# Kernel tuning notes

Measured on AMD Instinct MI355X. Metric: run time of the kernel, lower is better.

## Reference

```python
import jax, jax.numpy as jnp
import numpy as np

B, S, H, STATIC = 128, 128, 256, 2
BLOCKS = S // 2            # rotate_types = 2 for block_dim=2, allow_rot=True
DYN = 3 * BLOCKS           # dynamic channels: move / rotate_small / rotate_large


def setup_inputs() -> dict:
    key = jax.random.key(0)
    ks = jax.random.split(key, 16)
    p = lambda k, shape: (jax.random.normal(k, shape, jnp.float32) * 0.1)
    return {
        "static": jax.random.normal(ks[0], (B, STATIC + 1, S), jnp.float32),
        "dynamic": jnp.zeros((B, DYN, S), jnp.float32),
        "decoder_input": jax.random.normal(ks[1], (B, STATIC, 1), jnp.float32),
        # static/dynamic/decoder 1x1 conv encoders (weight [H, C_in], bias [H])
        "enc_s_W": p(ks[2], (H, STATIC)), "enc_s_b": p(ks[3], (H,)),
        "enc_d_W": p(ks[4], (H, DYN)),    "enc_d_b": p(ks[5], (H,)),
        "dec_W": p(ks[6], (H, STATIC)),   "dec_b": p(ks[7], (H,)),
        # single-layer GRU (torch layout: [3H, H] gates r,z,n)
        "gru_W_ih": p(ks[8], (3 * H, H)), "gru_W_hh": p(ks[9], (3 * H, H)),
        "gru_b_ih": p(ks[10], (3 * H,)),  "gru_b_hh": p(ks[11], (3 * H,)),
        # encoder attention and pointer heads: v [H], W [H, 3H]
        "attn_v": p(ks[12], (H,)), "attn_W": p(ks[13], (H, 3 * H)),
        "ptr_v": p(ks[14], (H,)),  "ptr_W": p(ks[15], (H, 3 * H)),
    }


def reference(static, dynamic, decoder_input,
              enc_s_W, enc_s_b, enc_d_W, enc_d_b, dec_W, dec_b,
              gru_W_ih, gru_W_hh, gru_b_ih, gru_b_hh,
              attn_v, attn_W, ptr_v, ptr_W):
    static_part = static[:, 1:, :]                                  # [B, STATIC, S]
    static_h = jnp.einsum('hi,bis->bhs', enc_s_W, static_part) + enc_s_b[None, :, None]
    dynamic_h = jnp.einsum('hi,bis->bhs', enc_d_W, dynamic) + enc_d_b[None, :, None]

    # initial mask from dynamic state (move + rotate feasibility)
    bn = dynamic.shape[1] // 3
    move = dynamic[:, :bn, :].sum(1)
    dyn_mask = dynamic[:, bn:2 * bn, :].sum(1) * dynamic[:, 2 * bn:3 * bn, :].sum(1) + move
    logmask = jnp.where(dyn_mask != 0, -jnp.inf, 0.0)               # log(current_mask), [B, S]

    hsz = gru_W_hh.shape[1]
    h0 = jnp.zeros((static.shape[0], hsz), static.dtype)            # GRU default zero state

    def gru_cell(x, h):
        gi = x @ gru_W_ih.T + gru_b_ih
        gh = h @ gru_W_hh.T + gru_b_hh
        ir, iz, inn = jnp.split(gi, 3, -1)
        hr, hz, hn = jnp.split(gh, 3, -1)
        r = jax.nn.sigmoid(ir + hr)
        z = jax.nn.sigmoid(iz + hz)
        n = jnp.tanh(inn + r * hn)
        return (1.0 - z) * n + z * h

    def step(carry, _):
        h_prev, dec_in = carry
        dec_h = jnp.einsum('hi,bi->bh', dec_W, dec_in[:, :, 0]) + dec_b   # decoder 1x1 conv
        h = gru_cell(dec_h, h_prev)                                       # rnn_out == new hidden
        rnn_b = jnp.broadcast_to(h[:, :, None], static_h.shape)
        hid = jnp.concatenate([static_h, dynamic_h, rnn_b], axis=1)       # [B, 3H, S]
        attn = jax.nn.softmax(
            jnp.einsum('h,bhs->bs', attn_v,
                       jnp.tanh(jnp.einsum('hk,bks->bhs', attn_W, hid))), axis=-1)
        context = jnp.einsum('bs,bhs->bh', attn, static_h)
        ctx_b = jnp.broadcast_to(context[:, :, None], static_h.shape)
        energy = jnp.concatenate([static_h, dynamic_h, ctx_b], axis=1)    # [B, 3H, S]
        logits = jnp.einsum('h,bhs->bs', ptr_v,
                            jnp.tanh(jnp.einsum('hk,bks->bhs', ptr_W, energy)))
        probs = jax.nn.softmax(logits + logmask, axis=-1)                 # [B, S]
        ptr = jnp.argmax(probs, axis=1)                                   # greedy (eval mode)
        logp = jnp.log(jnp.max(probs, axis=1))
        new_dec = jax.lax.stop_gradient(
            jnp.take_along_axis(static_part, ptr[:, None, None], axis=2))  # [B, STATIC, 1]
        return (h, new_dec), (ptr, logp)

    (_, _), (ptrs, logps) = jax.lax.scan(step, (h0, decoder_input), None,
                                         length=static_part.shape[2])
    tour_idx = ptrs.T    # [B, S]
    tour_logp = logps.T  # [B, S]
    return tour_idx, tour_logp
```

## Files before the change

### kernel.cpp

```cpp
#include <hip/hip_runtime.h>
#include <hip/hip_bf16.h>
#include <math.h>

#define BB   128
#define SS   128
#define HH   256
#define DYNN 192

#define OFF_FLAG  0
#define OFF_G     64
#define OFF_G0    (OFF_G + 1536)
#define OFF_M1A   (OFF_G0 + 768)
#define OFF_CA    (OFF_M1A + 512)
#define OFF_M1P   (OFF_CA + 256)
#define OFF_CP    (OFF_M1P + 512)
#define OFF_M3P   (OFF_CP + 256)
#define OFF_CP3   (OFF_M3P + 512)
#define OFF_LM    (OFF_CP3 + 256)
#define OFF_M2A   (OFF_LM + 16384)
#define OFF_M2P   (OFF_M2A + 49152)
#define OFF_BASEA (OFF_M2P + 49152)
#define OFF_BASEP (OFF_BASEA + 4194304)
#define OFF_END   (OFF_BASEP + 4194304)

__device__ __forceinline__ float tanh_fast(float x) {
    float e = __builtin_amdgcn_exp2f(x * 2.885390081777927f);
    return 1.0f - 2.0f * __builtin_amdgcn_rcpf(e + 1.0f);
}

__global__ void k1_logmask(const float* __restrict__ dyn, float* __restrict__ lm,
                           int* __restrict__ flag) {
    int g = blockIdx.x * 256 + threadIdx.x;
    if (g >= BB * SS) return;
    int b = g >> 7, s = g & 127;
    const float* p = dyn + (size_t)b * DYNN * SS + s;
    float mv = 0.f, m1 = 0.f, m2 = 0.f;
    bool nz = false;
    for (int i = 0; i < 64; ++i)        { float v = p[(size_t)i * SS]; mv += v; nz |= (v != 0.f); }
    for (int i = 64; i < 128; ++i)      { float v = p[(size_t)i * SS]; m1 += v; nz |= (v != 0.f); }
    for (int i = 128; i < 192; ++i)     { float v = p[(size_t)i * SS]; m2 += v; nz |= (v != 0.f); }
    float dm = m1 * m2 + mv;
    lm[g] = (dm != 0.f) ? -__builtin_inff() : 0.f;
    if (nz) atomicOr(flag, 1);
}

__global__ void k0a_folds(const float* __restrict__ Wih, const float* __restrict__ bih,
                          const float* __restrict__ dW,  const float* __restrict__ db,
                          const float* __restrict__ aW,  const float* __restrict__ pW,
                          const float* __restrict__ esW, const float* __restrict__ esb,
                          const float* __restrict__ edb, float* __restrict__ wsf) {
    int idx = blockIdx.x * 256 + threadIdx.x;
    float* G   = wsf + OFF_G;
    float* g0  = wsf + OFF_G0;
    float* M1a = wsf + OFF_M1A;
    float* ca  = wsf + OFF_CA;
    float* M1p = wsf + OFF_M1P;
    float* cp  = wsf + OFF_CP;
    float* M3p = wsf + OFF_M3P;
    float* cp3 = wsf + OFF_CP3;
    if (idx < 1536) {
        int r = idx >> 1, j = idx & 1;
        float a = 0.f;
        for (int k = 0; k < 256; ++k) a += Wih[r * 256 + k] * dW[k * 2 + j];
        G[idx] = a;
    } else if (idx < 2304) {
        int r = idx - 1536;
        float a = 0.f;
        for (int k = 0; k < 256; ++k) a += Wih[r * 256 + k] * db[k];
        g0[r] = a + bih[r];
    } else if (idx < 2816) {
        int t = idx - 2304; int h = t >> 1, j = t & 1;
        float a = 0.f;
        for (int k = 0; k < 256; ++k) a += aW[h * 768 + k] * esW[k * 2 + j];
        M1a[t] = a;
    } else if (idx < 3072) {
        int h = idx - 2816;
        float a = 0.f, b2 = 0.f;
        for (int k = 0; k < 256; ++k) a  += aW[h * 768 + k]       * esb[k];
        for (int k = 0; k < 256; ++k) b2 += aW[h * 768 + 256 + k] * edb[k];
        ca[h] = a + b2;
    } else if (idx < 3584) {
        int t = idx - 3072; int h = t >> 1, j = t & 1;
        float a = 0.f;
        for (int k = 0; k < 256; ++k) a += pW[h * 768 + k] * esW[k * 2 + j];
        M1p[t] = a;
    } else if (idx < 3840) {
        int h = idx - 3584;
        float a = 0.f, b2 = 0.f;
        for (int k = 0; k < 256; ++k) a  += pW[h * 768 + k]       * esb[k];
        for (int k = 0; k < 256; ++k) b2 += pW[h * 768 + 256 + k] * edb[k];
        cp[h] = a + b2;
    } else if (idx < 4352) {
        int t = idx - 3840; int h = t >> 1, j = t & 1;
        float a = 0.f;
        for (int k = 0; k < 256; ++k) a += pW[h * 768 + 512 + k] * esW[k * 2 + j];
        M3p[t] = a;
    } else if (idx < 4608) {
        int h = idx - 4352;
        float a = 0.f;
        for (int k = 0; k < 256; ++k) a += pW[h * 768 + 512 + k] * esb[k];
        cp3[h] = a;
    }
}

__global__ void k0b_m2(const float* __restrict__ aW, const float* __restrict__ pW,
                       const float* __restrict__ edW, float* __restrict__ wsf,
                       const int* __restrict__ flag) {
    if (*flag == 0) return;
    int idx = blockIdx.x * 256 + threadIdx.x;
    if (idx >= 2 * 49152) return;
    int which = idx / 49152;
    int t = idx % 49152;
    int h = t / DYNN, i = t % DYNN;
    const float* W = which ? pW : aW;
    float a = 0.f;
    for (int k = 0; k < 256; ++k) a += W[h * 768 + 256 + k] * edW[k * DYNN + i];
    wsf[(which ? OFF_M2P : OFF_M2A) + t] = a;
}

__global__ void k2_bases(const float* __restrict__ stat, const float* __restrict__ dyn,
                         float* __restrict__ wsf, const int* __restrict__ flag) {
    if (*flag == 0) return;
    __shared__ float col[DYNN];
    __shared__ float s01[2];
    const float* M1a = wsf + OFF_M1A; const float* ca  = wsf + OFF_CA;
    const float* M1p = wsf + OFF_M1P; const float* cp  = wsf + OFF_CP;
    const float* M2a = wsf + OFF_M2A; const float* M2p = wsf + OFF_M2P;
    float* basea = wsf + OFF_BASEA;   float* basep = wsf + OFF_BASEP;
    for (int pair = blockIdx.x; pair < BB * SS; pair += gridDim.x) {
        int b = pair >> 7, s = pair & 127;
        if (threadIdx.x < DYNN) col[threadIdx.x] = dyn[((size_t)b * DYNN + threadIdx.x) * SS + s];
        if (threadIdx.x == DYNN) {
            s01[0] = stat[((size_t)b * 3 + 1) * SS + s];
            s01[1] = stat[((size_t)b * 3 + 2) * SS + s];
        }
        __syncthreads();
        int h = threadIdx.x;
        float aa = fmaf(M1a[h * 2], s01[0], fmaf(M1a[h * 2 + 1], s01[1], ca[h]));
        float pp = fmaf(M1p[h * 2], s01[0], fmaf(M1p[h * 2 + 1], s01[1], cp[h]));
        for (int i = 0; i < DYNN; ++i) {
            aa = fmaf(M2a[h * DYNN + i], col[i], aa);
            pp = fmaf(M2p[h * DYNN + i], col[i], pp);
        }
        basea[((size_t)b * SS + s) * HH + h] = aa;
        basep[((size_t)b * SS + s) * HH + h] = pp;
        __syncthreads();
    }
}

__global__ __launch_bounds__(1024, 1) void k3_seq(
    const float* __restrict__ stat, const float* __restrict__ dec_inp,
    const float* __restrict__ Whh, const float* __restrict__ bhh_g,
    const float* __restrict__ aW, const float* __restrict__ av,
    const float* __restrict__ pv, const float* __restrict__ wsf,
    int allow_general, float* __restrict__ out) {
    const int b = blockIdx.x;
    const int tid = threadIdx.x;

    __shared__ float sh_h[256], sh_gh[768], sh_x[256], sh_t1[256];
    __shared__ float sh_sp0[128], sh_sp1[128], sh_lm[128];
    __shared__ float sh_M1a[512], sh_M1p[512], sh_M3p[512];
    __shared__ float sh_ca[256], sh_cp[256], sh_cp3[256];
    __shared__ float sh_G[1536], sh_g0[768], sh_bhh[768];
    __shared__ float sh_va[256], sh_vp[256];
    __shared__ float sh_a[128];
    __shared__ float sh_scal[8];

    const float* G_   = wsf + OFF_G;   const float* g0_  = wsf + OFF_G0;
    const float* M1a_ = wsf + OFF_M1A; const float* ca_  = wsf + OFF_CA;
    const float* M1p_ = wsf + OFF_M1P; const float* cp_  = wsf + OFF_CP;
    const float* M3p_ = wsf + OFF_M3P; const float* cp3_ = wsf + OFF_CP3;
    const float* lm_  = wsf + OFF_LM;
    const float* basea = wsf + OFF_BASEA;
    const float* basep = wsf + OFF_BASEP;
    const int* flag = (const int*)wsf;

    for (int i = tid; i < 1536; i += 1024) sh_G[i] = G_[i];
    for (int i = tid; i < 768; i += 1024) { sh_g0[i] = g0_[i]; sh_bhh[i] = bhh_g[i]; }
    for (int i = tid; i < 512; i += 1024) { sh_M1a[i] = M1a_[i]; sh_M1p[i] = M1p_[i]; sh_M3p[i] = M3p_[i]; }
    for (int i = tid; i < 256; i += 1024) {
        sh_ca[i] = ca_[i]; sh_cp[i] = cp_[i]; sh_cp3[i] = cp3_[i];
        sh_va[i] = av[i];  sh_vp[i] = pv[i];  sh_h[i] = 0.f;
    }
    for (int i = tid; i < 128; i += 1024) {
        sh_sp0[i] = stat[((size_t)b * 3 + 1) * SS + i];
        sh_sp1[i] = stat[((size_t)b * 3 + 2) * SS + i];
        sh_lm[i]  = lm_[b * SS + i];
    }
    if (tid == 0) { sh_scal[0] = dec_inp[b * 2 + 0]; sh_scal[1] = dec_inp[b * 2 + 1]; }
    const bool dz = (!allow_general) || (*flag == 0);
    __syncthreads();

    const int qw = tid >> 4;
    const int j  = tid & 15;

    for (int t = 0; t < SS; ++t) {
        for (int r = qw; r < 768; r += 64) {
            const float4* Wr = (const float4*)(Whh + (size_t)r * 256);
            const float4* xx = (const float4*)sh_x; (void)xx;
            float acc = 0.f;
            #pragma unroll
            for (int i2 = 0; i2 < 4; ++i2) {
                float4 w = Wr[j + 16 * i2];
                float4 x = ((const float4*)sh_h)[j + 16 * i2];
                acc = fmaf(w.x, x.x, fmaf(w.y, x.y, fmaf(w.z, x.z, fmaf(w.w, x.w, acc))));
            }
            acc += __shfl_xor(acc, 1, 16); acc += __shfl_xor(acc, 2, 16);
            acc += __shfl_xor(acc, 4, 16); acc += __shfl_xor(acc, 8, 16);
            if (j == 0) sh_gh[r] = acc + sh_bhh[r];
        }
        __syncthreads();

        if (tid < 256) {
            int k = tid;
            float d0 = sh_scal[0], d1 = sh_scal[1];
            float gr = fmaf(sh_G[k * 2],          d0, fmaf(sh_G[k * 2 + 1],          d1, sh_g0[k]));
            float gz = fmaf(sh_G[(k + 256) * 2],  d0, fmaf(sh_G[(k + 256) * 2 + 1],  d1, sh_g0[k + 256]));
            float gn = fmaf(sh_G[(k + 512) * 2],  d0, fmaf(sh_G[(k + 512) * 2 + 1],  d1, sh_g0[k + 512]));
            float r = 1.f / (1.f + expf(-(gr + sh_gh[k])));
            float z = 1.f / (1.f + expf(-(gz + sh_gh[k + 256])));
            float n = tanhf(gn + r * sh_gh[k + 512]);
            float hn = (1.f - z) * n + z * sh_h[k];
            sh_x[k] = hn;
            sh_h[k] = hn;
        }
        __syncthreads();

        for (int r = qw; r < 256; r += 64) {
            const float4* Wr = (const float4*)(aW + (size_t)r * 768 + 512);
            float acc = 0.f;
            #pragma unroll
            for (int i2 = 0; i2 < 4; ++i2) {
                float4 w = Wr[j + 16 * i2];
                float4 x = ((const float4*)sh_x)[j + 16 * i2];
                acc = fmaf(w.x, x.x, fmaf(w.y, x.y, fmaf(w.z, x.z, fmaf(w.w, x.w, acc))));
            }
            acc += __shfl_xor(acc, 1, 16); acc += __shfl_xor(acc, 2, 16);
            acc += __shfl_xor(acc, 4, 16); acc += __shfl_xor(acc, 8, 16);
            if (j == 0) sh_t1[r] = acc + (dz ? sh_ca[r] : 0.f);
        }
        __syncthreads();

        {
            int s = tid >> 3, g = tid & 7;
            float acc = 0.f;
            if (dz) {
                float s0 = sh_sp0[s], s1 = sh_sp1[s];
                #pragma unroll 8
                for (int i = g; i < 256; i += 8) {
                    float arg = fmaf(sh_M1a[i * 2], s0, fmaf(sh_M1a[i * 2 + 1], s1, sh_t1[i]));
                    acc = fmaf(sh_va[i], tanh_fast(arg), acc);
                }
            } else {
                const float* bb = basea + ((size_t)b * SS + s) * HH;
                #pragma unroll 8
                for (int i = g; i < 256; i += 8)
                    acc = fmaf(sh_va[i], tanh_fast(bb[i] + sh_t1[i]), acc);
            }
            acc += __shfl_xor(acc, 1, 8); acc += __shfl_xor(acc, 2, 8); acc += __shfl_xor(acc, 4, 8);
            if (g == 0) sh_a[s] = acc;
        }
        __syncthreads();

        if (tid < 64) {
            float v0 = sh_a[tid], v1 = sh_a[tid + 64];
            float m = fmaxf(v0, v1);
            for (int msk = 1; msk < 64; msk <<= 1) m = fmaxf(m, __shfl_xor(m, msk, 64));
            float e0 = expf(v0 - m), e1 = expf(v1 - m);
            float S = e0 + e1;
            float c0 = e0 * sh_sp0[tid] + e1 * sh_sp0[tid + 64];
            float c1 = e0 * sh_sp1[tid] + e1 * sh_sp1[tid + 64];
            for (int msk = 1; msk < 64; msk <<= 1) {
                S  += __shfl_xor(S,  msk, 64);
                c0 += __shfl_xor(c0, msk, 64);
                c1 += __shfl_xor(c1, msk, 64);
            }
            if (tid == 0) { sh_scal[2] = c0 / S; sh_scal[3] = c1 / S; }
        }
        __syncthreads();

        if (tid < 256) {
            int k = tid;
            float C0 = sh_scal[2], C1 = sh_scal[3];
            float v = fmaf(sh_M3p[k * 2], C0, fmaf(sh_M3p[k * 2 + 1], C1, sh_cp3[k]));
            sh_t1[k] = v + (dz ? sh_cp[k] : 0.f);
        }
        __syncthreads();

        {
            int s = tid >> 3, g = tid & 7;
            float acc = 0.f;
            if (dz) {
                float s0 = sh_sp0[s], s1 = sh_sp1[s];
                #pragma unroll 8
                for (int i = g; i < 256; i += 8) {
                    float arg = fmaf(sh_M1p[i * 2], s0, fmaf(sh_M1p[i * 2 + 1], s1, sh_t1[i]));
                    acc = fmaf(sh_vp[i], tanh_fast(arg), acc);
                }
            } else {
                const float* bb = basep + ((size_t)b * SS + s) * HH;
                #pragma unroll 8
                for (int i = g; i < 256; i += 8)
                    acc = fmaf(sh_vp[i], tanh_fast(bb[i] + sh_t1[i]), acc);
            }
            acc += __shfl_xor(acc, 1, 8); acc += __shfl_xor(acc, 2, 8); acc += __shfl_xor(acc, 4, 8);
            if (g == 0) sh_a[s] = acc;
        }
        __syncthreads();

        if (tid < 64) {
            float l0 = sh_a[tid] + sh_lm[tid];
            float l1 = sh_a[tid + 64] + sh_lm[tid + 64];
            float v; int idx;
            if (l0 >= l1) { v = l0; idx = tid; } else { v = l1; idx = tid + 64; }
            for (int msk = 1; msk < 64; msk <<= 1) {
                float ov = __shfl_xor(v, msk, 64);
                int   oi = __shfl_xor(idx, msk, 64);
                if (ov > v || (ov == v && oi < idx)) { v = ov; idx = oi; }
            }
            float S = expf(l0 - v) + expf(l1 - v);
            for (int msk = 1; msk < 64; msk <<= 1) S += __shfl_xor(S, msk, 64);
            if (tid == 0) {
                out[b * SS + t] = (float)idx;
                out[BB * SS + b * SS + t] = -logf(S);
                sh_scal[0] = sh_sp0[idx];
                sh_scal[1] = sh_sp1[idx];
            }
        }
        __syncthreads();
    }
}

extern "C" void kernel_launch(void* const* d_in, const int* in_sizes, int n_in,
                              void* d_out, int out_size, void* d_ws, size_t ws_size,
                              hipStream_t stream) {
    const float* stat  = (const float*)d_in[0];
    const float* dyn   = (const float*)d_in[1];
    const float* decin = (const float*)d_in[2];
    const float* esW   = (const float*)d_in[3];
    const float* esb   = (const float*)d_in[4];
    const float* edW   = (const float*)d_in[5];
    const float* edb   = (const float*)d_in[6];
    const float* dW    = (const float*)d_in[7];
    const float* db    = (const float*)d_in[8];
    const float* Wih   = (const float*)d_in[9];
    const float* Whh   = (const float*)d_in[10];
    const float* bih   = (const float*)d_in[11];
    const float* bhh   = (const float*)d_in[12];
    const float* av    = (const float*)d_in[13];
    const float* aW    = (const float*)d_in[14];
    const float* pv    = (const float*)d_in[15];
    const float* pW    = (const float*)d_in[16];
    float* wsf = (float*)d_ws;
    int* flag  = (int*)d_ws;
    float* out = (float*)d_out;

    int allow_general = (ws_size >= (size_t)OFF_END * 4) ? 1 : 0;

    hipMemsetAsync(d_ws, 0, 64 * 4, stream);
    hipLaunchKernelGGL(k1_logmask, dim3(64), dim3(256), 0, stream, dyn, wsf + OFF_LM, flag);
    hipLaunchKernelGGL(k0a_folds, dim3(18), dim3(256), 0, stream,
                       Wih, bih, dW, db, aW, pW, esW, esb, edb, wsf);
    if (allow_general) {
        hipLaunchKernelGGL(k0b_m2, dim3(384), dim3(256), 0, stream, aW, pW, edW, wsf, flag);
        hipLaunchKernelGGL(k2_bases, dim3(256), dim3(256), 0, stream, stat, dyn, wsf, flag);
    }
    hipLaunchKernelGGL(k3_seq, dim3(128), dim3(1024), 0, stream,
                       stat, decin, Whh, bhh, aW, av, pv, wsf, allow_general, out);
}
```

Baseline: 1.927 ms.

## Overlap next-step GRU hidden matvec with attention/pointer chain via warp specialization

Splits the 1024-thread block into two halves. The first 512 threads compute the recurrent W_hh·h matvec for the next step, with part of W_hh held in registers. The other 512 threads run the attention, context and pointer chain for the current step, synchronizing among themselves with a shared-memory counter barrier (atomic plus sleep) instead of __syncthreads. The aim is to take the GRU matvec off the serial critical path and cut block-wide barriers per step from seven to two. The costs are higher register pressure, less parallelism per stage, and spin-wait overhead on the custom barrier.

```diff
diff --git a/kernel.cpp b/kernel.cpp
--- a/kernel.cpp
+++ b/kernel.cpp
@@ -6,6 +6,7 @@
 #define SS   128
 #define HH   256
 #define DYNN 192
+#define NC   4
 
 #define OFF_FLAG  0
 #define OFF_G     64
@@ -26,6 +27,13 @@
 __device__ __forceinline__ float tanh_fast(float x) {
     float e = __builtin_amdgcn_exp2f(x * 2.885390081777927f);
     return 1.0f - 2.0f * __builtin_amdgcn_rcpf(e + 1.0f);
+}
+
+__device__ __forceinline__ void ybar(int* cnt, bool arrive, int target) {
+    if (arrive && (threadIdx.x & 63) == 0)
+        __hip_atomic_fetch_add(cnt, 1, __ATOMIC_RELEASE, __HIP_MEMORY_SCOPE_WORKGROUP);
+    while (__hip_atomic_load(cnt, __ATOMIC_ACQUIRE, __HIP_MEMORY_SCOPE_WORKGROUP) < target)
+        __builtin_amdgcn_s_sleep(1);
 }
 
 __global__ void k1_logmask(const float* __restrict__ dyn, float* __restrict__ lm,
@@ -157,14 +165,14 @@
     const int b = blockIdx.x;
     const int tid = threadIdx.x;
 
-    __shared__ float sh_h[256], sh_gh[768], sh_x[256], sh_t1[256];
+    __shared__ float sh_gh[768], sh_hv[256], sh_t1[256], sh_a[128];
     __shared__ float sh_sp0[128], sh_sp1[128], sh_lm[128];
     __shared__ float sh_M1a[512], sh_M1p[512], sh_M3p[512];
     __shared__ float sh_ca[256], sh_cp[256], sh_cp3[256];
     __shared__ float sh_G[1536], sh_g0[768], sh_bhh[768];
     __shared__ float sh_va[256], sh_vp[256];
-    __shared__ float sh_a[128];
-    __shared__ float sh_scal[8];
+    __shared__ float sh_scal[4];
+    __shared__ int ycnt;
 
     const float* G_   = wsf + OFF_G;   const float* g0_  = wsf + OFF_G0;
     const float* M1a_ = wsf + OFF_M1A; const float* ca_  = wsf + OFF_CA;
@@ -176,41 +184,42 @@
     const int* flag = (const int*)wsf;
 
     for (int i = tid; i < 1536; i += 1024) sh_G[i] = G_[i];
-    for (int i = tid; i < 768; i += 1024) { sh_g0[i] = g0_[i]; sh_bhh[i] = bhh_g[i]; }
+    for (int i = tid; i < 768; i += 1024) {
+        sh_g0[i] = g0_[i];
+        float bv = bhh_g[i];
+        sh_bhh[i] = bv;
+        sh_gh[i] = bv;
+    }
     for (int i = tid; i < 512; i += 1024) { sh_M1a[i] = M1a_[i]; sh_M1p[i] = M1p_[i]; sh_M3p[i] = M3p_[i]; }
     for (int i = tid; i < 256; i += 1024) {
         sh_ca[i] = ca_[i]; sh_cp[i] = cp_[i]; sh_cp3[i] = cp3_[i];
-        sh_va[i] = av[i];  sh_vp[i] = pv[i];  sh_h[i] = 0.f;
+        sh_va[i] = av[i];  sh_vp[i] = pv[i];  sh_hv[i] = 0.f;
     }
     for (int i = tid; i < 128; i += 1024) {
         sh_sp0[i] = stat[((size_t)b * 3 + 1) * SS + i];
         sh_sp1[i] = stat[((size_t)b * 3 + 2) * SS + i];
         sh_lm[i]  = lm_[b * SS + i];
     }
-    if (tid == 0) { sh_scal[0] = dec_inp[b * 2 + 0]; sh_scal[1] = dec_inp[b * 2 + 1]; }
+    if (tid == 0) {
+        sh_scal[0] = dec_inp[b * 2 + 0];
+        sh_scal[1] = dec_inp[b * 2 + 1];
+        ycnt = 0;
+    }
     const bool dz = (!allow_general) || (*flag == 0);
+
+    const int xg = tid >> 4, xj = tid & 15;
+    float4 cw[NC][4];
+    if (tid < 512) {
+        #pragma unroll
+        for (int k = 0; k < NC; ++k) {
+            const float4* Wr = (const float4*)(Whh + (size_t)(xg + 32 * k) * 256);
+            #pragma unroll
+            for (int i2 = 0; i2 < 4; ++i2) cw[k][i2] = Wr[xj + 16 * i2];
+        }
+    }
     __syncthreads();
 
-    const int qw = tid >> 4;
-    const int j  = tid & 15;
-
     for (int t = 0; t < SS; ++t) {
-        for (int r = qw; r < 768; r += 64) {
-            const float4* Wr = (const float4*)(Whh + (size_t)r * 256);
-            const float4* xx = (const float4*)sh_x; (void)xx;
-            float acc = 0.f;
-            #pragma unroll
-            for (int i2 = 0; i2 < 4; ++i2) {
-                float4 w = Wr[j + 16 * i2];
-                float4 x = ((const float4*)sh_h)[j + 16 * i2];
-                acc = fmaf(w.x, x.x, fmaf(w.y, x.y, fmaf(w.z, x.z, fmaf(w.w, x.w, acc))));
-            }
-            acc += __shfl_xor(acc, 1, 16); acc += __shfl_xor(acc, 2, 16);
-            acc += __shfl_xor(acc, 4, 16); acc += __shfl_xor(acc, 8, 16);
-            if (j == 0) sh_gh[r] = acc + sh_bhh[r];
-        }
-        __syncthreads();
-
         if (tid < 256) {
             int k = tid;
             float d0 = sh_scal[0], d1 = sh_scal[1];
@@ -220,111 +229,149 @@
             float r = 1.f / (1.f + expf(-(gr + sh_gh[k])));
             float z = 1.f / (1.f + expf(-(gz + sh_gh[k + 256])));
             float n = tanhf(gn + r * sh_gh[k + 512]);
-            float hn = (1.f - z) * n + z * sh_h[k];
-            sh_x[k] = hn;
-            sh_h[k] = hn;
+            sh_hv[k] = (1.f - z) * n + z * sh_hv[k];
         }
         __syncthreads();
 
-        for (int r = qw; r < 256; r += 64) {
-            const float4* Wr = (const float4*)(aW + (size_t)r * 768 + 512);
-            float acc = 0.f;
-            #pragma unroll
-            for (int i2 = 0; i2 < 4; ++i2) {
-                float4 w = Wr[j + 16 * i2];
-                float4 x = ((const float4*)sh_x)[j + 16 * i2];
-                acc = fmaf(w.x, x.x, fmaf(w.y, x.y, fmaf(w.z, x.z, fmaf(w.w, x.w, acc))));
-            }
-            acc += __shfl_xor(acc, 1, 16); acc += __shfl_xor(acc, 2, 16);
-            acc += __shfl_xor(acc, 4, 16); acc += __shfl_xor(acc, 8, 16);
-            if (j == 0) sh_t1[r] = acc + (dz ? sh_ca[r] : 0.f);
-        }
-        __syncthreads();
-
-        {
-            int s = tid >> 3, g = tid & 7;
-            float acc = 0.f;
-            if (dz) {
-                float s0 = sh_sp0[s], s1 = sh_sp1[s];
-                #pragma unroll 8
-                for (int i = g; i < 256; i += 8) {
-                    float arg = fmaf(sh_M1a[i * 2], s0, fmaf(sh_M1a[i * 2 + 1], s1, sh_t1[i]));
-                    acc = fmaf(sh_va[i], tanh_fast(arg), acc);
-                }
+        if (tid < 512) {
+            if (t < SS - 1) {
+                #pragma unroll
+                for (int k = 0; k < NC; ++k) {
+                    float acc = 0.f;
+                    #pragma unroll
+                    for (int i2 = 0; i2 < 4; ++i2) {
+                        float4 w = cw[k][i2];
+                        float4 x = ((const float4*)sh_hv)[xj + 16 * i2];
+                        acc = fmaf(w.x, x.x, fmaf(w.y, x.y, fmaf(w.z, x.z, fmaf(w.w, x.w, acc))));
+                    }
+                    acc += __shfl_xor(acc, 1, 16); acc += __shfl_xor(acc, 2, 16);
+                    acc += __shfl_xor(acc, 4, 16); acc += __shfl_xor(acc, 8, 16);
+                    if (xj == 0) { int r = xg + 32 * k; sh_gh[r] = acc + sh_bhh[r]; }
+                }
+                for (int k = NC; k < 24; ++k) {
+                    int r = xg + 32 * k;
+                    const float4* Wr = (const float4*)(Whh + (size_t)r * 256);
+                    float acc = 0.f;
+                    #pragma unroll
+                    for (int i2 = 0; i2 < 4; ++i2) {
+                        float4 w = Wr[xj + 16 * i2];
+                        float4 x = ((const float4*)sh_hv)[xj + 16 * i2];
+                        acc = fmaf(w.x, x.x, fmaf(w.y, x.y, fmaf(w.z, x.z, fmaf(w.w, x.w, acc))));
+                    }
+                    acc += __shfl_xor(acc, 1, 16); acc += __shfl_xor(acc, 2, 16);
+                    acc += __shfl_xor(acc, 4, 16); acc += __shfl_xor(acc, 8, 16);
+                    if (xj == 0) sh_gh[r] = acc + sh_bhh[r];
+                }
+            }
+        } else {
+            const int yt = tid - 512;
+            const int ybase = t * 25;
+
+            {
+                const int yq = yt >> 4, yj = yt & 15;
+                for (int r = yq; r < 256; r += 32) {
+                    const float4* Wr = (const float4*)(aW + (size_t)r * 768 + 512);
+                    float acc = 0.f;
+                    #pragma unroll
+                    for (int i2 = 0; i2 < 4; ++i2) {
+                        float4 w = Wr[yj + 16 * i2];
+                        float4 x = ((const float4*)sh_hv)[yj + 16 * i2];
+                        acc = fmaf(w.x, x.x, fmaf(w.y, x.y, fmaf(w.z, x.z, fmaf(w.w, x.w, acc))));
+                    }
+                    acc += __shfl_xor(acc, 1, 16); acc += __shfl_xor(acc, 2, 16);
+                    acc += __shfl_xor(acc, 4, 16); acc += __shfl_xor(acc, 8, 16);
+                    if (yj == 0) sh_t1[r] = acc + (dz ? sh_ca[r] : 0.f);
+                }
+            }
+            ybar(&ycnt, true, ybase + 8);
+
+            {
+                int s = yt >> 2, g = yt & 3;
+                float acc = 0.f;
+                if (dz) {
+                    float s0 = sh_sp0[s], s1 = sh_sp1[s];
+                    #pragma unroll 8
+                    for (int i = g; i < 256; i += 4) {
+                        float arg = fmaf(sh_M1a[i * 2], s0, fmaf(sh_M1a[i * 2 + 1], s1, sh_t1[i]));
+                        acc = fmaf(sh_va[i], tanh_fast(arg), acc);
+                    }
+                } else {
+                    const float* bb = basea + ((size_t)b * SS + s) * HH;
+                    #pragma unroll 8
+                    for (int i = g; i < 256; i += 4)
+                        acc = fmaf(sh_va[i], tanh_fast(bb[i] + sh_t1[i]), acc);
+                }
+                acc += __shfl_xor(acc, 1, 4); acc += __shfl_xor(acc, 2, 4);
+                if (g == 0) sh_a[s] = acc;
+            }
+            ybar(&ycnt, true, ybase + 16);
+
+            if (yt < 64) {
+                int lane = yt;
+                float v0 = sh_a[lane], v1 = sh_a[lane + 64];
+                float m = fmaxf(v0, v1);
+                for (int msk = 1; msk < 64; msk <<= 1) m = fmaxf(m, __shfl_xor(m, msk, 64));
+                float e0 = expf(v0 - m), e1 = expf(v1 - m);
+                float S = e0 + e1;
+                float c0 = e0 * sh_sp0[lane] + e1 * sh_sp0[lane + 64];
+                float c1 = e0 * sh_sp1[lane] + e1 * sh_sp1[lane + 64];
+                for (int msk = 1; msk < 64; msk <<= 1) {
+                    S  += __shfl_xor(S,  msk, 64);
+                    c0 += __shfl_xor(c0, msk, 64);
+                    c1 += __shfl_xor(c1, msk, 64);
+                }
+                float C0 = c0 / S, C1 = c1 / S;
+                #pragma unroll
+                for (int q = 0; q < 4; ++q) {
+                    int k2 = lane + 64 * q;
+                    float v = fmaf(sh_M3p[k2 * 2], C0, fmaf(sh_M3p[k2 * 2 + 1], C1, sh_cp3[k2]));
+                    sh_t1[k2] = v + (dz ? sh_cp[k2] : 0.f);
+                }
+                ybar(&ycnt, true, ybase + 17);
             } else {
-                const float* bb = basea + ((size_t)b * SS + s) * HH;
-                #pragma unroll 8
-                for (int i = g; i < 256; i += 8)
-                    acc = fmaf(sh_va[i], tanh_fast(bb[i] + sh_t1[i]), acc);
-            }
-            acc += __shfl_xor(acc, 1, 8); acc += __shfl_xor(acc, 2, 8); acc += __shfl_xor(acc, 4, 8);
-            if (g == 0) sh_a[s] = acc;
-        }
-        __syncthreads();
-
-        if (tid < 64) {
-            float v0 = sh_a[tid], v1 = sh_a[tid + 64];
-            float m = fmaxf(v0, v1);
-            for (int msk = 1; msk < 64; msk <<= 1) m = fmaxf(m, __shfl_xor(m, msk, 64));
-            float e0 = expf(v0 - m), e1 = expf(v1 - m);
-            float S = e0 + e1;
-            float c0 = e0 * sh_sp0[tid] + e1 * sh_sp0[tid + 64];
-            float c1 = e0 * sh_sp1[tid] + e1 * sh_sp1[tid + 64];
-            for (int msk = 1; msk < 64; msk <<= 1) {
-                S  += __shfl_xor(S,  msk, 64);
-                c0 += __shfl_xor(c0, msk, 64);
-                c1 += __shfl_xor(c1, msk, 64);
-            }
-            if (tid == 0) { sh_scal[2] = c0 / S; sh_scal[3] = c1 / S; }
-        }
-        __syncthreads();
-
-        if (tid < 256) {
-            int k = tid;
-            float C0 = sh_scal[2], C1 = sh_scal[3];
-            float v = fmaf(sh_M3p[k * 2], C0, fmaf(sh_M3p[k * 2 + 1], C1, sh_cp3[k]));
-            sh_t1[k] = v + (dz ? sh_cp[k] : 0.f);
-        }
-        __syncthreads();
-
-        {
-            int s = tid >> 3, g = tid & 7;
-            float acc = 0.f;
-            if (dz) {
-                float s0 = sh_sp0[s], s1 = sh_sp1[s];
-                #pragma unroll 8
-                for (int i = g; i < 256; i += 8) {
-                    float arg = fmaf(sh_M1p[i * 2], s0, fmaf(sh_M1p[i * 2 + 1], s1, sh_t1[i]));
-                    acc = fmaf(sh_vp[i], tanh_fast(arg), acc);
-                }
-            } else {
-                const float* bb = basep + ((size_t)b * SS + s) * HH;
-                #pragma unroll 8
-                for (int i = g; i < 256; i += 8)
-                    acc = fmaf(sh_vp[i], tanh_fast(bb[i] + sh_t1[i]), acc);
-            }
-            acc += __shfl_xor(acc, 1, 8); acc += __shfl_xor(acc, 2, 8); acc += __shfl_xor(acc, 4, 8);
-            if (g == 0) sh_a[s] = acc;
-        }
-        __syncthreads();
-
-        if (tid < 64) {
-            float l0 = sh_a[tid] + sh_lm[tid];
-            float l1 = sh_a[tid + 64] + sh_lm[tid + 64];
-            float v; int idx;
-            if (l0 >= l1) { v = l0; idx = tid; } else { v = l1; idx = tid + 64; }
-            for (int msk = 1; msk < 64; msk <<= 1) {
-                float ov = __shfl_xor(v, msk, 64);
-                int   oi = __shfl_xor(idx, msk, 64);
-                if (ov > v || (ov == v && oi < idx)) { v = ov; idx = oi; }
-            }
-            float S = expf(l0 - v) + expf(l1 - v);
-            for (int msk = 1; msk < 64; msk <<= 1) S += __shfl_xor(S, msk, 64);
-            if (tid == 0) {
-                out[b * SS + t] = (float)idx;
-                out[BB * SS + b * SS + t] = -logf(S);
-                sh_scal[0] = sh_sp0[idx];
-                sh_scal[1] = sh_sp1[idx];
+                ybar(&ycnt, false, ybase + 17);
+            }
+
+            {
+                int s = yt >> 2, g = yt & 3;
+                float acc = 0.f;
+                if (dz) {
+                    float s0 = sh_sp0[s], s1 = sh_sp1[s];
+                    #pragma unroll 8
+                    for (int i = g; i < 256; i += 4) {
+                        float arg = fmaf(sh_M1p[i * 2], s0, fmaf(sh_M1p[i * 2 + 1], s1, sh_t1[i]));
+                        acc = fmaf(sh_vp[i], tanh_fast(arg), acc);
+                    }
+                } else {
+                    const float* bb = basep + ((size_t)b * SS + s) * HH;
+                    #pragma unroll 8
+                    for (int i = g; i < 256; i += 4)
+                        acc = fmaf(sh_vp[i], tanh_fast(bb[i] + sh_t1[i]), acc);
+                }
+                acc += __shfl_xor(acc, 1, 4); acc += __shfl_xor(acc, 2, 4);
+                if (g == 0) sh_a[s] = acc;
+            }
+            ybar(&ycnt, true, ybase + 25);
+
+            if (yt < 64) {
+                int lane = yt;
+                float l0 = sh_a[lane] + sh_lm[lane];
+                float l1 = sh_a[lane + 64] + sh_lm[lane + 64];
+                float v; int idx;
+                if (l0 >= l1) { v = l0; idx = lane; } else { v = l1; idx = lane + 64; }
+                for (int msk = 1; msk < 64; msk <<= 1) {
+                    float ov = __shfl_xor(v, msk, 64);
+                    int   oi = __shfl_xor(idx, msk, 64);
+                    if (ov > v || (ov == v && oi < idx)) { v = ov; idx = oi; }
+                }
+                float S = expf(l0 - v) + expf(l1 - v);
+                for (int msk = 1; msk < 64; msk <<= 1) S += __shfl_xor(S, msk, 64);
+                if (lane == 0) {
+                    out[b * SS + t] = (float)idx;
+                    out[BB * SS + b * SS + t] = -logf(S);
+                    sh_scal[0] = sh_sp0[idx];
+                    sh_scal[1] = sh_sp1[idx];
+                }
             }
         }
         __syncthreads();
```

After: 2.330 ms. +20.9%, slower.
